# Kernel optimization log

Measured on AMD Instinct MI355X. Metric: run time of the kernel, lower is better.

## Reference

```python
import jax, jax.numpy as jnp
import numpy as np

H = 256           # lstm_hidden_dim
D_IN = 22         # input_dim
H1, H2, H3 = 1024, 512, 1024
RRI = 2
N_R = N_L = 384


def _lstm_dir(x, Wih, Whh, b, reverse):
    # x: [T, D]; Wih: [4H, D]; Whh: [4H, H]; b: [4H] (bih+bhh). PyTorch gate order i,f,g,o.
    xs = x[::-1] if reverse else x
    pre = xs @ Wih.T + b                       # [T, 4H] input projection hoisted out of scan
    hdim = Whh.shape[1]

    def step(carry, p):
        h, c = carry
        g = p + h @ Whh.T
        i, f, gg, o = jnp.split(g, 4)
        i = jax.nn.sigmoid(i); f = jax.nn.sigmoid(f)
        gg = jnp.tanh(gg); o = jax.nn.sigmoid(o)
        c = f * c + i * gg
        h = o * jnp.tanh(c)
        return (h, c), h

    h0 = jnp.zeros((hdim,), x.dtype)
    _, hs = jax.lax.scan(step, (h0, h0), pre)
    return hs[::-1] if reverse else hs


def _bilstm(x, Wih0, Whh0, bih0, bhh0, Wih1, Whh1, bih1, bhh1):
    # 2-layer bidirectional LSTM (dropout between layers is identity in eval).
    b0 = bih0 + bhh0
    x1 = jnp.concatenate([_lstm_dir(x, Wih0[0], Whh0[0], b0[0], False),
                          _lstm_dir(x, Wih0[1], Whh0[1], b0[1], True)], axis=-1)
    b1 = bih1 + bhh1
    return jnp.concatenate([_lstm_dir(x1, Wih1[0], Whh1[0], b1[0], False),
                            _lstm_dir(x1, Wih1[1], Whh1[1], b1[1], True)], axis=-1)


def _mlp(h, W1, b1, W2, b2):
    h1 = jax.nn.relu(h @ W1.T + b1)
    return jax.nn.relu(h1 @ W2.T + b2)   # [N, H2]


def setup_inputs() -> dict:
    key = jax.random.key(0)
    ks = jax.random.split(key, 20)
    s = 0.05
    f = lambda k, shp: (jax.random.normal(k, shp, dtype=jnp.float32) * s)
    return {
        "v_r": jax.random.normal(ks[0], (N_R, D_IN), dtype=jnp.float32),
        "v_l": jax.random.normal(ks[1], (N_L, D_IN), dtype=jnp.float32),
        # LSTM layer 0 (input D_IN), stacked over 2 directions
        "Wih0": f(ks[2], (2, 4 * H, D_IN)),
        "Whh0": f(ks[3], (2, 4 * H, H)),
        "bih0": f(ks[4], (2, 4 * H)),
        "bhh0": f(ks[5], (2, 4 * H)),
        # LSTM layer 1 (input 2H)
        "Wih1": f(ks[6], (2, 4 * H, 2 * H)),
        "Whh1": f(ks[7], (2, 4 * H, H)),
        "bih1": f(ks[8], (2, 4 * H)),
        "bhh1": f(ks[9], (2, 4 * H)),
        # MLP heads
        "W1": f(ks[10], (H1, 2 * H)), "b1": f(ks[11], (H1,)),
        "W2": f(ks[12], (H2, H1)),    "b2": f(ks[13], (H2,)),
        "W3": f(ks[14], (H3, 2 * H2)), "b3": f(ks[15], (H3,)),
        "Wout": f(ks[16], (RRI, H3)), "bout": f(ks[17], (RRI,)),
    }


def reference(v_r, v_l, Wih0, Whh0, bih0, bhh0, Wih1, Whh1, bih1, bhh1,
              W1, b1, W2, b2, W3, b3, Wout, bout):
    out_r = _bilstm(v_r, Wih0, Whh0, bih0, bhh0, Wih1, Whh1, bih1, bhh1)  # [Nr, 2H]
    out_l = _bilstm(v_l, Wih0, Whh0, bih0, bhh0, Wih1, Whh1, bih1, bhh1)  # [Nl, 2H]
    hr = _mlp(out_r, W1, b1, W2, b2)   # [Nr, H2]
    hl = _mlp(out_l, W1, b1, W2, b2)   # [Nl, H2]
    # Original: 0.5*(Linear3([hr_i, hl_j]) + Linear3([hl_j, hr_i])) built via huge
    # repeat()s; exactly equal to u_r[i] + u_l[j] + b3 with the split weight sum.
    d2 = hr.shape[-1]
    W3s = (W3[:, :d2] + W3[:, d2:]).T            # [H2, H3]
    u_r = 0.5 * (hr @ W3s)                       # [Nr, H3]
    u_l = 0.5 * (hl @ W3s)                       # [Nl, H3]
    conv = jax.nn.relu(u_r[:, None, :] + u_l[None, :, :] + b3)  # [Nr, Nl, H3]
    v_in = conv.reshape(-1, conv.shape[-1])      # [Nr*Nl, H3], i_r-major like the torch loop
    logits = v_in @ Wout.T + bout                # [Nr*Nl, rri_size]
    return jax.nn.log_softmax(logits, axis=-1)
```

## Files before the change

### kernel.cpp

```cpp
#include <hip/hip_runtime.h>
#include <math.h>


typedef _Float16 half2_t __attribute__((ext_vector_type(2)));

__device__ __forceinline__ float fast_sig(float x) {
    float e = __expf(-x);
    return __builtin_amdgcn_rcpf(1.f + e);
}
__device__ __forceinline__ float fast_tanh(float x) {
    x = fminf(fmaxf(x, -30.f), 30.f);
    float e = __expf(2.f * x);
    return (e - 1.f) * __builtin_amdgcn_rcpf(e + 1.f);
}

__global__ __launch_bounds__(256) void prep_kernel(
    const float* __restrict__ bih0, const float* __restrict__ bhh0,
    const float* __restrict__ bih1, const float* __restrict__ bhh1,
    const float* __restrict__ W3,   const float* __restrict__ Wout,
    float* __restrict__ b0sum, float* __restrict__ b1sum,
    float* __restrict__ W3sum, float* __restrict__ woutT)
{
    int idx = blockIdx.x * 256 + threadIdx.x;
    int stride = gridDim.x * 256;
    if (idx < 2048) {
        b0sum[idx] = bih0[idx] + bhh0[idx];
        b1sum[idx] = bih1[idx] + bhh1[idx];
        woutT[idx] = Wout[(idx & 1) * 1024 + (idx >> 1)];
    }
    for (int i = idx; i < 1024 * 512; i += stride) {
        int n = i >> 9, k = i & 511;
        W3sum[i] = W3[n * 1024 + k] + W3[n * 1024 + 512 + k];
    }
}

__global__ __launch_bounds__(256) void proj0_kernel(
    const float* __restrict__ v_r, const float* __restrict__ v_l,
    const float* __restrict__ Wih0, const float* __restrict__ b0sum,
    float* __restrict__ pre0)
{
    int t = blockIdx.x;
    int sd = blockIdx.y;
    int seq = sd >> 1, dir = sd & 1;
    const float* x = (seq ? v_l : v_r) + t * 22;
    __shared__ float sx[22];
    if (threadIdx.x < 22) sx[threadIdx.x] = x[threadIdx.x];
    __syncthreads();
#pragma unroll
    for (int q = 0; q < 4; ++q) {
        int o = q * 256 + threadIdx.x;
        const float* wr = Wih0 + (size_t)(dir * 1024 + o) * 22;
        float acc = b0sum[dir * 1024 + o];
#pragma unroll
        for (int d = 0; d < 22; ++d) acc += sx[d] * wr[d];
        pre0[((size_t)sd * 384 + t) * 1024 + o] = acc;
    }
}

__global__ __launch_bounds__(512) void lstm_rec_kernel(
    const float* __restrict__ Whh,
    const float* __restrict__ pre,
    float* __restrict__ out,
    unsigned long long* pub,
    int layer)
{
    const int b = blockIdx.x;
    const int chain = b & 7;
    const int w = b >> 3;
    if (chain >= 4) return;
    const int seq = chain >> 1, dir = chain & 1;
    const int tid = threadIdx.x;
    const int ks = tid & 7;
    const int jloc = tid >> 3;
    const int jj = (w << 6) + jloc;

    __shared__ __align__(16) float4 hh4[2][40];

    float wA[64];
#pragma unroll
    for (int g = 0; g < 4; ++g) {
        const float* wr = Whh + (((size_t)(dir * 1024 + g * 256 + jj)) << 8) + (ks << 5);
#pragma unroll
        for (int q = 0; q < 16; ++q) {
            float2 v = *(const float2*)(wr + 2 * q);
            half2_t h2; h2.x = (_Float16)v.x; h2.y = (_Float16)v.y;
            wA[g * 16 + q] = __builtin_bit_cast(float, h2);
        }
    }
#pragma unroll
    for (int q = 0; q < 64; ++q) asm volatile("" : "+v"(wA[q]));

    if (tid < 320) ((float*)hh4)[tid] = 0.f;
    float cstate = 0.f;
    __syncthreads();

    for (int s = 0; s < 384; ++s) {
        const int t = dir ? (383 - s) : s;
        const float* pre_t = (layer == 0)
            ? pre + ((size_t)(seq * 2 + dir) * 384 + t) * 1024
            : pre + (((size_t)(seq * 384 + t)) * 2 + dir) * 1024;
        float pv = (ks < 4) ? pre_t[(ks << 8) + jj] : 0.f;

        const int par = s & 1, pn = par ^ 1;
        if (s > 0 && ks >= 6) {
            int cid = (jloc << 1) | (ks - 6);
            if (cid < 96) {
                int peer = cid >> 5;
                int p = cid & 31;
                int wp = (w + 1 + peer) & 3;
                int P = (wp << 5) + p;
                const unsigned long long* src =
                    &pub[((size_t)chain * 2 + par) * 128 + P];
                const unsigned expect = (unsigned)s;
                unsigned long long v =
                    __hip_atomic_load(src, __ATOMIC_RELAXED, __HIP_MEMORY_SCOPE_AGENT);
                if ((unsigned)(v >> 32) != expect) {
                    for (int it = 0; it < 65536; ++it) {
                        __builtin_amdgcn_s_sleep(1);
                        v = __hip_atomic_load(src, __ATOMIC_RELAXED, __HIP_MEMORY_SCOPE_AGENT);
                        if ((unsigned)(v >> 32) == expect) break;
                    }
                }
                ((half2_t*)&hh4[par][0])[(P >> 4) * 20 + (P & 15)] =
                    __builtin_bit_cast(half2_t, (unsigned)v);
            }
        }
        __syncthreads();

        const float4* hb = &hh4[par][ks * 5];
        float4 hl0 = hb[0], hl1 = hb[1], hl2 = hb[2], hl3 = hb[3];
        const float4 hls[4] = {hl0, hl1, hl2, hl3};
        float a0 = 0.f, a1 = 0.f, a2 = 0.f, a3 = 0.f;
#pragma unroll
        for (int m = 0; m < 4; ++m) {
            const float he[4] = {hls[m].x, hls[m].y, hls[m].z, hls[m].w};
#pragma unroll
            for (int e = 0; e < 4; ++e) {
                half2_t hv = __builtin_bit_cast(half2_t, he[e]);
                int q = 4 * m + e;
                a0 = __builtin_amdgcn_fdot2(__builtin_bit_cast(half2_t, wA[q]),      hv, a0, false);
                a1 = __builtin_amdgcn_fdot2(__builtin_bit_cast(half2_t, wA[16 + q]), hv, a1, false);
                a2 = __builtin_amdgcn_fdot2(__builtin_bit_cast(half2_t, wA[32 + q]), hv, a2, false);
                a3 = __builtin_amdgcn_fdot2(__builtin_bit_cast(half2_t, wA[48 + q]), hv, a3, false);
            }
        }
        a0 += (ks == 0) ? pv : 0.f;
        a1 += (ks == 1) ? pv : 0.f;
        a2 += (ks == 2) ? pv : 0.f;
        a3 += (ks == 3) ? pv : 0.f;
#pragma unroll
        for (int d = 1; d < 8; d <<= 1) {
            a0 += __shfl_xor(a0, d);
            a1 += __shfl_xor(a1, d);
            a2 += __shfl_xor(a2, d);
            a3 += __shfl_xor(a3, d);
        }

        float iv = fast_sig(a0);
        float fv = fast_sig(a1);
        float gv = fast_tanh(a2);
        float ov = fast_sig(a3);
        cstate = fv * cstate + iv * gv;
        float h = ov * fast_tanh(cstate);

        unsigned hb16 = (unsigned)__builtin_bit_cast(unsigned short, (_Float16)h);
        unsigned nb = (unsigned)__shfl_xor((int)hb16, 8);
        if (ks == 0) {
            ((unsigned short*)&hh4[pn][0])[(jj >> 5) * 40 + (jj & 31)] =
                (unsigned short)hb16;
            if ((jloc & 1) == 0) {
                unsigned payload = (hb16 & 0xffffu) | (nb << 16);
                int P = (w << 5) + (jloc >> 1);
                unsigned long long pk =
                    ((unsigned long long)(unsigned)(s + 1) << 32) | payload;
                __hip_atomic_store(&pub[((size_t)chain * 2 + pn) * 128 + P], pk,
                                   __ATOMIC_RELAXED, __HIP_MEMORY_SCOPE_AGENT);
            }
        }
        if (ks == 1) {
            out[((size_t)seq * 384 + t) * 512 + dir * 256 + jj] = h;
        }
        __syncthreads();
    }
}

__global__ __launch_bounds__(256) void gemm_nt_kernel(
    const float* __restrict__ A, const float* __restrict__ W,
    const float* __restrict__ bias, float* __restrict__ C,
    int M, int N, int K, float scale, int do_relu)
{
    __shared__ float As[32][68];
    __shared__ float Ws[32][68];
    const int tid = threadIdx.x;
    const int n0 = blockIdx.x * 64, m0 = blockIdx.y * 64;
    const int lr = tid >> 2;
    const int lk = (tid & 3) * 8;
    const int tm = tid >> 4, tn = tid & 15;
    float acc[4][4];
#pragma unroll
    for (int i = 0; i < 4; ++i)
#pragma unroll
        for (int j = 0; j < 4; ++j) acc[i][j] = 0.f;

    for (int kc = 0; kc < K; kc += 32) {
        float4 a0 = *(const float4*)(A + (size_t)(m0 + lr) * K + kc + lk);
        float4 a1 = *(const float4*)(A + (size_t)(m0 + lr) * K + kc + lk + 4);
        float4 w0 = *(const float4*)(W + (size_t)(n0 + lr) * K + kc + lk);
        float4 w1 = *(const float4*)(W + (size_t)(n0 + lr) * K + kc + lk + 4);
        __syncthreads();
        As[lk + 0][lr] = a0.x; As[lk + 1][lr] = a0.y; As[lk + 2][lr] = a0.z; As[lk + 3][lr] = a0.w;
        As[lk + 4][lr] = a1.x; As[lk + 5][lr] = a1.y; As[lk + 6][lr] = a1.z; As[lk + 7][lr] = a1.w;
        Ws[lk + 0][lr] = w0.x; Ws[lk + 1][lr] = w0.y; Ws[lk + 2][lr] = w0.z; Ws[lk + 3][lr] = w0.w;
        Ws[lk + 4][lr] = w1.x; Ws[lk + 5][lr] = w1.y; Ws[lk + 6][lr] = w1.z; Ws[lk + 7][lr] = w1.w;
        __syncthreads();
#pragma unroll
        for (int kk = 0; kk < 32; ++kk) {
            float4 av = *(const float4*)&As[kk][tm * 4];
            float4 wv = *(const float4*)&Ws[kk][tn * 4];
            acc[0][0] += av.x * wv.x; acc[0][1] += av.x * wv.y; acc[0][2] += av.x * wv.z; acc[0][3] += av.x * wv.w;
            acc[1][0] += av.y * wv.x; acc[1][1] += av.y * wv.y; acc[1][2] += av.y * wv.z; acc[1][3] += av.y * wv.w;
            acc[2][0] += av.z * wv.x; acc[2][1] += av.z * wv.y; acc[2][2] += av.z * wv.z; acc[2][3] += av.z * wv.w;
            acc[3][0] += av.w * wv.x; acc[3][1] += av.w * wv.y; acc[3][2] += av.w * wv.z; acc[3][3] += av.w * wv.w;
        }
    }
    float4 bv = make_float4(0.f, 0.f, 0.f, 0.f);
    if (bias) bv = *(const float4*)(bias + n0 + tn * 4);
#pragma unroll
    for (int i = 0; i < 4; ++i) {
        int m = m0 + tm * 4 + i;
        float4 v;
        v.x = scale * acc[i][0] + bv.x;
        v.y = scale * acc[i][1] + bv.y;
        v.z = scale * acc[i][2] + bv.z;
        v.w = scale * acc[i][3] + bv.w;
        if (do_relu) {
            v.x = fmaxf(v.x, 0.f); v.y = fmaxf(v.y, 0.f);
            v.z = fmaxf(v.z, 0.f); v.w = fmaxf(v.w, 0.f);
        }
        *(float4*)(C + (size_t)m * N + n0 + tn * 4) = v;
    }
}

__global__ __launch_bounds__(256) void pairwise_kernel(
    const float* __restrict__ u,
    const float* __restrict__ woutT,
    const float* __restrict__ bout,
    float* __restrict__ out)
{
    __shared__ float Ur[32][132];
    __shared__ float Ul[32][132];
    __shared__ float Wo[256];
    const int tid = threadIdx.x;
    const int j0 = blockIdx.x * 32, i0 = blockIdx.y * 32;
    const int ii = tid >> 4, jj = tid & 15;
    const int il0 = ii, il1 = ii + 16;
    const int jl0 = jj, jl1 = jj + 16;
    float acc000 = 0.f, acc001 = 0.f, acc010 = 0.f, acc011 = 0.f;
    float acc100 = 0.f, acc101 = 0.f, acc110 = 0.f, acc111 = 0.f;
    const int lrw = tid >> 3;
    const int lcb = (tid & 7) * 16;

    for (int cc = 0; cc < 1024; cc += 128) {
        __syncthreads();
#pragma unroll
        for (int q = 0; q < 4; ++q) {
            *(float4*)&Ur[lrw][lcb + 4 * q] =
                *(const float4*)(u + (size_t)(i0 + lrw) * 1024 + cc + lcb + 4 * q);
            *(float4*)&Ul[lrw][lcb + 4 * q] =
                *(const float4*)(u + (size_t)(384 + j0 + lrw) * 1024 + cc + lcb + 4 * q);
        }
        if (tid < 128)
            *(float2*)&Wo[tid * 2] = *(const float2*)(woutT + (size_t)(cc + tid) * 2);
        __syncthreads();

        for (int c = 0; c < 128; c += 4) {
            float4 a0  = *(const float4*)&Ur[il0][c];
            float4 a1  = *(const float4*)&Ur[il1][c];
            float4 b0v = *(const float4*)&Ul[jl0][c];
            float4 b1v = *(const float4*)&Ul[jl1][c];
            float4 wA4 = *(const float4*)&Wo[c * 2];
            float4 wB4 = *(const float4*)&Wo[c * 2 + 4];
#define PW_STEP(AX, W0, W1)                                   \
            { float rr;                                       \
              rr = fmaxf(a0.AX + b0v.AX, 0.f); acc000 += rr*(W0); acc001 += rr*(W1); \
              rr = fmaxf(a0.AX + b1v.AX, 0.f); acc010 += rr*(W0); acc011 += rr*(W1); \
              rr = fmaxf(a1.AX + b0v.AX, 0.f); acc100 += rr*(W0); acc101 += rr*(W1); \
              rr = fmaxf(a1.AX + b1v.AX, 0.f); acc110 += rr*(W0); acc111 += rr*(W1); }
            PW_STEP(x, wA4.x, wA4.y)
            PW_STEP(y, wA4.z, wA4.w)
            PW_STEP(z, wB4.x, wB4.y)
            PW_STEP(w, wB4.z, wB4.w)
#undef PW_STEP
        }
    }
    float2 bo = *(const float2*)bout;
    float pa[2][2][2] = {{{acc000, acc001}, {acc010, acc011}},
                         {{acc100, acc101}, {acc110, acc111}}};
#pragma unroll
    for (int pi = 0; pi < 2; ++pi)
#pragma unroll
        for (int pj = 0; pj < 2; ++pj) {
            float l0 = pa[pi][pj][0] + bo.x;
            float l1 = pa[pi][pj][1] + bo.y;
            float m = fmaxf(l0, l1);
            float lse = m + logf(expf(l0 - m) + expf(l1 - m));
            int ig = i0 + ii + 16 * pi;
            int jg = j0 + jj + 16 * pj;
            float2 o2; o2.x = l0 - lse; o2.y = l1 - lse;
            *(float2*)(out + ((size_t)ig * 384 + jg) * 2) = o2;
        }
}

extern "C" void kernel_launch(void* const* d_in, const int* in_sizes, int n_in,
                              void* d_out, int out_size, void* d_ws, size_t ws_size,
                              hipStream_t stream)
{
    const float* v_r  = (const float*)d_in[0];
    const float* v_l  = (const float*)d_in[1];
    const float* Wih0 = (const float*)d_in[2];
    const float* Whh0 = (const float*)d_in[3];
    const float* bih0 = (const float*)d_in[4];
    const float* bhh0 = (const float*)d_in[5];
    const float* Wih1 = (const float*)d_in[6];
    const float* Whh1 = (const float*)d_in[7];
    const float* bih1 = (const float*)d_in[8];
    const float* bhh1 = (const float*)d_in[9];
    const float* W1   = (const float*)d_in[10];
    const float* b1   = (const float*)d_in[11];
    const float* W2   = (const float*)d_in[12];
    const float* b2   = (const float*)d_in[13];
    const float* W3   = (const float*)d_in[14];
    const float* b3   = (const float*)d_in[15];
    const float* Wout = (const float*)d_in[16];
    const float* bout = (const float*)d_in[17];
    float* out = (float*)d_out;

    float* ws = (float*)d_ws;
    size_t off = 0;
    float* b0sum = ws + off; off += 2048;
    float* b1sum = ws + off; off += 2048;
    float* W3sum = ws + off; off += 1024 * 512;
    float* woutT = ws + off; off += 2048;
    float* pre0  = ws + off; off += (size_t)4 * 384 * 1024;
    float* out0  = ws + off; off += (size_t)2 * 384 * 512;
    float* pre1  = ws + off; off += (size_t)768 * 2048;
    float* out1  = ws + off; off += (size_t)2 * 384 * 512;
    float* h1    = ws + off; off += (size_t)768 * 1024;
    float* h2    = ws + off; off += (size_t)768 * 512;
    float* u     = ws + off; off += (size_t)768 * 1024;
    unsigned long long* pub0 = (unsigned long long*)(ws + off); off += 4 * 2 * 128 * 2;
    unsigned long long* pub1 = (unsigned long long*)(ws + off); off += 4 * 2 * 128 * 2;

    prep_kernel<<<512, 256, 0, stream>>>(bih0, bhh0, bih1, bhh1, W3, Wout,
                                         b0sum, b1sum, W3sum, woutT);
    proj0_kernel<<<dim3(384, 4), 256, 0, stream>>>(v_r, v_l, Wih0, b0sum, pre0);
    lstm_rec_kernel<<<32, 512, 0, stream>>>(Whh0, pre0, out0, pub0, 0);
    gemm_nt_kernel<<<dim3(2048 / 64, 768 / 64), 256, 0, stream>>>(
        out0, Wih1, b1sum, pre1, 768, 2048, 512, 1.f, 0);
    lstm_rec_kernel<<<32, 512, 0, stream>>>(Whh1, pre1, out1, pub1, 1);
    gemm_nt_kernel<<<dim3(1024 / 64, 768 / 64), 256, 0, stream>>>(
        out1, W1, b1, h1, 768, 1024, 512, 1.f, 1);
    gemm_nt_kernel<<<dim3(512 / 64, 768 / 64), 256, 0, stream>>>(
        h1, W2, b2, h2, 768, 512, 1024, 1.f, 1);
    gemm_nt_kernel<<<dim3(1024 / 64, 384 / 64), 256, 0, stream>>>(
        h2, W3sum, b3, u, 384, 1024, 512, 0.5f, 0);
    gemm_nt_kernel<<<dim3(1024 / 64, 384 / 64), 256, 0, stream>>>(
        h2 + (size_t)384 * 512, W3sum, nullptr, u + (size_t)384 * 1024, 384, 1024, 512, 0.5f, 0);
    pairwise_kernel<<<dim3(12, 12), 256, 0, stream>>>(u, woutT, bout, out);
}
```

Baseline: 1.213 ms.

## Interleave two sequences per LSTM recurrence block to hide cross-block latency

Each recurrence block now processes both sequences (r and l) of the same direction in alternation, so only 8 active blocks run instead of 16, and each block holds one copy of the Whh weights. While one chain computes, the poll for the other chain's peer h values is already in flight, and a speculative prefetch load is issued before the wait. This is meant to hide inter-block handoff latency behind the other chain's compute. The cost is double the per-step compute and barriers in each block, on half as many CUs.

```diff
diff --git a/kernel.cpp b/kernel.cpp
--- a/kernel.cpp
+++ b/kernel.cpp
@@ -65,16 +65,17 @@
     int layer)
 {
     const int b = blockIdx.x;
-    const int chain = b & 7;
+    const int dir = b & 7;
     const int w = b >> 3;
-    if (chain >= 4) return;
-    const int seq = chain >> 1, dir = chain & 1;
+    if (dir >= 2) return;
     const int tid = threadIdx.x;
     const int ks = tid & 7;
     const int jloc = tid >> 3;
     const int jj = (w << 6) + jloc;
-
-    __shared__ __align__(16) float4 hh4[2][40];
+    const int cA = dir;
+    const int cB = 2 + dir;
+
+    __shared__ __align__(16) float4 hh4[2][2][40];
 
     float wA[64];
 #pragma unroll
@@ -90,95 +91,182 @@
 #pragma unroll
     for (int q = 0; q < 64; ++q) asm volatile("" : "+v"(wA[q]));
 
-    if (tid < 320) ((float*)hh4)[tid] = 0.f;
-    float cstate = 0.f;
+    ((float*)hh4)[tid] = 0.f;
+    if (tid < 128) ((float*)hh4)[512 + tid] = 0.f;
+    float cstA = 0.f, cstB = 0.f;
+
+    const int cid = (jloc << 1) | (ks & 1);
+    const bool poller = (ks >= 6) && (cid < 96);
+    int P = 0;
+    const unsigned long long* srcA = nullptr;
+    const unsigned long long* srcB = nullptr;
+    if (poller) {
+        int peer = cid >> 5, pr = cid & 31;
+        int wp = (w + 1 + peer) & 3;
+        P = (wp << 5) + pr;
+    }
+    unsigned long long pktA = 0, pktB = 0;
     __syncthreads();
 
     for (int s = 0; s < 384; ++s) {
         const int t = dir ? (383 - s) : s;
-        const float* pre_t = (layer == 0)
-            ? pre + ((size_t)(seq * 2 + dir) * 384 + t) * 1024
-            : pre + (((size_t)(seq * 384 + t)) * 2 + dir) * 1024;
-        float pv = (ks < 4) ? pre_t[(ks << 8) + jj] : 0.f;
+        const float* preA = (layer == 0)
+            ? pre + ((size_t)(0 * 2 + dir) * 384 + t) * 1024
+            : pre + (((size_t)(0 * 384 + t)) * 2 + dir) * 1024;
+        const float* preB = (layer == 0)
+            ? pre + ((size_t)(1 * 2 + dir) * 384 + t) * 1024
+            : pre + (((size_t)(1 * 384 + t)) * 2 + dir) * 1024;
+        float pvA = (ks < 4) ? preA[(ks << 8) + jj] : 0.f;
+        float pvB = (ks < 4) ? preB[(ks << 8) + jj] : 0.f;
 
         const int par = s & 1, pn = par ^ 1;
-        if (s > 0 && ks >= 6) {
-            int cid = (jloc << 1) | (ks - 6);
-            if (cid < 96) {
-                int peer = cid >> 5;
-                int p = cid & 31;
-                int wp = (w + 1 + peer) & 3;
-                int P = (wp << 5) + p;
-                const unsigned long long* src =
-                    &pub[((size_t)chain * 2 + par) * 128 + P];
-                const unsigned expect = (unsigned)s;
-                unsigned long long v =
-                    __hip_atomic_load(src, __ATOMIC_RELAXED, __HIP_MEMORY_SCOPE_AGENT);
-                if ((unsigned)(v >> 32) != expect) {
-                    for (int it = 0; it < 65536; ++it) {
-                        __builtin_amdgcn_s_sleep(1);
-                        v = __hip_atomic_load(src, __ATOMIC_RELAXED, __HIP_MEMORY_SCOPE_AGENT);
-                        if ((unsigned)(v >> 32) == expect) break;
-                    }
-                }
-                ((half2_t*)&hh4[par][0])[(P >> 4) * 20 + (P & 15)] =
-                    __builtin_bit_cast(half2_t, (unsigned)v);
-            }
-        }
-        __syncthreads();
-
-        const float4* hb = &hh4[par][ks * 5];
-        float4 hl0 = hb[0], hl1 = hb[1], hl2 = hb[2], hl3 = hb[3];
-        const float4 hls[4] = {hl0, hl1, hl2, hl3};
-        float a0 = 0.f, a1 = 0.f, a2 = 0.f, a3 = 0.f;
-#pragma unroll
-        for (int m = 0; m < 4; ++m) {
-            const float he[4] = {hls[m].x, hls[m].y, hls[m].z, hls[m].w};
-#pragma unroll
-            for (int e = 0; e < 4; ++e) {
-                half2_t hv = __builtin_bit_cast(half2_t, he[e]);
-                int q = 4 * m + e;
-                a0 = __builtin_amdgcn_fdot2(__builtin_bit_cast(half2_t, wA[q]),      hv, a0, false);
-                a1 = __builtin_amdgcn_fdot2(__builtin_bit_cast(half2_t, wA[16 + q]), hv, a1, false);
-                a2 = __builtin_amdgcn_fdot2(__builtin_bit_cast(half2_t, wA[32 + q]), hv, a2, false);
-                a3 = __builtin_amdgcn_fdot2(__builtin_bit_cast(half2_t, wA[48 + q]), hv, a3, false);
-            }
-        }
-        a0 += (ks == 0) ? pv : 0.f;
-        a1 += (ks == 1) ? pv : 0.f;
-        a2 += (ks == 2) ? pv : 0.f;
-        a3 += (ks == 3) ? pv : 0.f;
-#pragma unroll
-        for (int d = 1; d < 8; d <<= 1) {
-            a0 += __shfl_xor(a0, d);
-            a1 += __shfl_xor(a1, d);
-            a2 += __shfl_xor(a2, d);
-            a3 += __shfl_xor(a3, d);
-        }
-
-        float iv = fast_sig(a0);
-        float fv = fast_sig(a1);
-        float gv = fast_tanh(a2);
-        float ov = fast_sig(a3);
-        cstate = fv * cstate + iv * gv;
-        float h = ov * fast_tanh(cstate);
-
-        unsigned hb16 = (unsigned)__builtin_bit_cast(unsigned short, (_Float16)h);
-        unsigned nb = (unsigned)__shfl_xor((int)hb16, 8);
-        if (ks == 0) {
-            ((unsigned short*)&hh4[pn][0])[(jj >> 5) * 40 + (jj & 31)] =
-                (unsigned short)hb16;
-            if ((jloc & 1) == 0) {
-                unsigned payload = (hb16 & 0xffffu) | (nb << 16);
-                int P = (w << 5) + (jloc >> 1);
-                unsigned long long pk =
-                    ((unsigned long long)(unsigned)(s + 1) << 32) | payload;
-                __hip_atomic_store(&pub[((size_t)chain * 2 + pn) * 128 + P], pk,
-                                   __ATOMIC_RELAXED, __HIP_MEMORY_SCOPE_AGENT);
-            }
-        }
-        if (ks == 1) {
-            out[((size_t)seq * 384 + t) * 512 + dir * 256 + jj] = h;
+
+        if (s > 0 && poller) {
+            const unsigned long long* src =
+                &pub[((size_t)cA * 2 + par) * 128 + P];
+            if ((unsigned)(pktA >> 32) != (unsigned)s) {
+                for (int it = 0; it < 65536; ++it) {
+                    __builtin_amdgcn_s_sleep(1);
+                    pktA = __hip_atomic_load(src, __ATOMIC_RELAXED, __HIP_MEMORY_SCOPE_AGENT);
+                    if ((unsigned)(pktA >> 32) == (unsigned)s) break;
+                }
+            }
+            ((half2_t*)&hh4[0][par][0])[(P >> 4) * 20 + (P & 15)] =
+                __builtin_bit_cast(half2_t, (unsigned)pktA);
+        }
+        __syncthreads();
+
+        if (s > 0 && poller)
+            pktB = __hip_atomic_load(&pub[((size_t)cB * 2 + par) * 128 + P],
+                                     __ATOMIC_RELAXED, __HIP_MEMORY_SCOPE_AGENT);
+
+        {
+            const float4* hb = &hh4[0][par][ks * 5];
+            float4 hl0 = hb[0], hl1 = hb[1], hl2 = hb[2], hl3 = hb[3];
+            const float4 hls[4] = {hl0, hl1, hl2, hl3};
+            float a0 = 0.f, a1 = 0.f, a2 = 0.f, a3 = 0.f;
+#pragma unroll
+            for (int m = 0; m < 4; ++m) {
+                const float he[4] = {hls[m].x, hls[m].y, hls[m].z, hls[m].w};
+#pragma unroll
+                for (int e = 0; e < 4; ++e) {
+                    half2_t hv = __builtin_bit_cast(half2_t, he[e]);
+                    int q = 4 * m + e;
+                    a0 = __builtin_amdgcn_fdot2(__builtin_bit_cast(half2_t, wA[q]),      hv, a0, false);
+                    a1 = __builtin_amdgcn_fdot2(__builtin_bit_cast(half2_t, wA[16 + q]), hv, a1, false);
+                    a2 = __builtin_amdgcn_fdot2(__builtin_bit_cast(half2_t, wA[32 + q]), hv, a2, false);
+                    a3 = __builtin_amdgcn_fdot2(__builtin_bit_cast(half2_t, wA[48 + q]), hv, a3, false);
+                }
+            }
+            a0 += (ks == 0) ? pvA : 0.f;
+            a1 += (ks == 1) ? pvA : 0.f;
+            a2 += (ks == 2) ? pvA : 0.f;
+            a3 += (ks == 3) ? pvA : 0.f;
+#pragma unroll
+            for (int d = 1; d < 8; d <<= 1) {
+                a0 += __shfl_xor(a0, d);
+                a1 += __shfl_xor(a1, d);
+                a2 += __shfl_xor(a2, d);
+                a3 += __shfl_xor(a3, d);
+            }
+            float iv = fast_sig(a0);
+            float fv = fast_sig(a1);
+            float gv = fast_tanh(a2);
+            float ov = fast_sig(a3);
+            cstA = fv * cstA + iv * gv;
+            float h = ov * fast_tanh(cstA);
+
+            unsigned hb16 = (unsigned)__builtin_bit_cast(unsigned short, (_Float16)h);
+            unsigned nb = (unsigned)__shfl_xor((int)hb16, 8);
+            if (ks == 0) {
+                ((unsigned short*)&hh4[0][pn][0])[(jj >> 5) * 40 + (jj & 31)] =
+                    (unsigned short)hb16;
+                if ((jloc & 1) == 0) {
+                    unsigned payload = (hb16 & 0xffffu) | (nb << 16);
+                    int Pw = (w << 5) + (jloc >> 1);
+                    unsigned long long pk =
+                        ((unsigned long long)(unsigned)(s + 1) << 32) | payload;
+                    __hip_atomic_store(&pub[((size_t)cA * 2 + pn) * 128 + Pw], pk,
+                                       __ATOMIC_RELAXED, __HIP_MEMORY_SCOPE_AGENT);
+                }
+            }
+            if (ks == 1) {
+                out[((size_t)0 * 384 + t) * 512 + dir * 256 + jj] = h;
+            }
+        }
+
+        if (s > 0 && poller) {
+            const unsigned long long* src =
+                &pub[((size_t)cB * 2 + par) * 128 + P];
+            if ((unsigned)(pktB >> 32) != (unsigned)s) {
+                for (int it = 0; it < 65536; ++it) {
+                    __builtin_amdgcn_s_sleep(1);
+                    pktB = __hip_atomic_load(src, __ATOMIC_RELAXED, __HIP_MEMORY_SCOPE_AGENT);
+                    if ((unsigned)(pktB >> 32) == (unsigned)s) break;
+                }
+            }
+            ((half2_t*)&hh4[1][par][0])[(P >> 4) * 20 + (P & 15)] =
+                __builtin_bit_cast(half2_t, (unsigned)pktB);
+        }
+        __syncthreads();
+
+        if (poller)
+            pktA = __hip_atomic_load(&pub[((size_t)cA * 2 + pn) * 128 + P],
+                                     __ATOMIC_RELAXED, __HIP_MEMORY_SCOPE_AGENT);
+
+        {
+            const float4* hb = &hh4[1][par][ks * 5];
+            float4 hl0 = hb[0], hl1 = hb[1], hl2 = hb[2], hl3 = hb[3];
+            const float4 hls[4] = {hl0, hl1, hl2, hl3};
+            float a0 = 0.f, a1 = 0.f, a2 = 0.f, a3 = 0.f;
+#pragma unroll
+            for (int m = 0; m < 4; ++m) {
+                const float he[4] = {hls[m].x, hls[m].y, hls[m].z, hls[m].w};
+#pragma unroll
+                for (int e = 0; e < 4; ++e) {
+                    half2_t hv = __builtin_bit_cast(half2_t, he[e]);
+                    int q = 4 * m + e;
+                    a0 = __builtin_amdgcn_fdot2(__builtin_bit_cast(half2_t, wA[q]),      hv, a0, false);
+                    a1 = __builtin_amdgcn_fdot2(__builtin_bit_cast(half2_t, wA[16 + q]), hv, a1, false);
+                    a2 = __builtin_amdgcn_fdot2(__builtin_bit_cast(half2_t, wA[32 + q]), hv, a2, false);
+                    a3 = __builtin_amdgcn_fdot2(__builtin_bit_cast(half2_t, wA[48 + q]), hv, a3, false);
+                }
+            }
+            a0 += (ks == 0) ? pvB : 0.f;
+            a1 += (ks == 1) ? pvB : 0.f;
+            a2 += (ks == 2) ? pvB : 0.f;
+            a3 += (ks == 3) ? pvB : 0.f;
+#pragma unroll
+            for (int d = 1; d < 8; d <<= 1) {
+                a0 += __shfl_xor(a0, d);
+                a1 += __shfl_xor(a1, d);
+                a2 += __shfl_xor(a2, d);
+                a3 += __shfl_xor(a3, d);
+            }
+            float iv = fast_sig(a0);
+            float fv = fast_sig(a1);
+            float gv = fast_tanh(a2);
+            float ov = fast_sig(a3);
+            cstB = fv * cstB + iv * gv;
+            float h = ov * fast_tanh(cstB);
+
+            unsigned hb16 = (unsigned)__builtin_bit_cast(unsigned short, (_Float16)h);
+            unsigned nb = (unsigned)__shfl_xor((int)hb16, 8);
+            if (ks == 0) {
+                ((unsigned short*)&hh4[1][pn][0])[(jj >> 5) * 40 + (jj & 31)] =
+                    (unsigned short)hb16;
+                if ((jloc & 1) == 0) {
+                    unsigned payload = (hb16 & 0xffffu) | (nb << 16);
+                    int Pw = (w << 5) + (jloc >> 1);
+                    unsigned long long pk =
+                        ((unsigned long long)(unsigned)(s + 1) << 32) | payload;
+                    __hip_atomic_store(&pub[((size_t)cB * 2 + pn) * 128 + Pw], pk,
+                                       __ATOMIC_RELAXED, __HIP_MEMORY_SCOPE_AGENT);
+                }
+            }
+            if (ks == 1) {
+                out[((size_t)1 * 384 + t) * 512 + dir * 256 + jj] = h;
+            }
         }
         __syncthreads();
     }
```

Result: slower. 1.839 ms (+51.6%).
